# Performance work log

Measured on AMD Instinct MI355X. Metric: run time of the kernel, lower is better.

Reference implementation:

```python
import jax, jax.numpy as jnp
import numpy as np

GRID = 128      # voxel grid extent per axis
NUM_BATCH = 4
N_PER = 25000   # points per scene (unique voxels)
C = 128
K = 32          # number of classes in probs
HEADS = 8
SCALE = 1.0


def setup_inputs() -> dict:
    key = jax.random.key(0)
    ks = jax.random.split(key, 12)
    N = NUM_BATCH * N_PER
    # unique voxel coordinates per scene (submanifold conv assumes no duplicate sites)
    coords_list = []
    for b in range(NUM_BATCH):
        flat = jax.random.permutation(jax.random.fold_in(ks[0], b), GRID ** 3)[:N_PER]
        xyz = jnp.stack([flat // (GRID * GRID), (flat // GRID) % GRID, flat % GRID], axis=1)
        bcol = jnp.full((N_PER, 1), b)
        coords_list.append(jnp.concatenate([bcol, xyz], axis=1))
    coords = jnp.concatenate(coords_list, axis=0).astype(jnp.int32)  # [N,4] = (b,x,y,z)
    feats = jax.random.normal(ks[1], (N, C), jnp.float32)
    probs = jax.random.normal(ks[2], (N, K), jnp.float32)
    conv_w = jax.random.normal(ks[3], (27, C, C), jnp.float32) * (1.0 / np.sqrt(27 * C))
    bn_gamma = 1.0 + 0.1 * jax.random.normal(ks[4], (C,), jnp.float32)
    bn_beta = 0.1 * jax.random.normal(ks[5], (C,), jnp.float32)
    in_proj_w = jax.random.normal(ks[6], (3 * C, C), jnp.float32) / np.sqrt(C)
    in_proj_b = 0.01 * jax.random.normal(ks[7], (3 * C,), jnp.float32)
    out_proj_w = jax.random.normal(ks[8], (C, C), jnp.float32) / np.sqrt(C)
    out_proj_b = 0.01 * jax.random.normal(ks[9], (C,), jnp.float32)
    bottleneck_w = jax.random.normal(ks[10], (C, 2 * C), jnp.float32) / np.sqrt(2 * C)
    return {"feats": feats, "probs": probs, "conv_w": conv_w, "bn_gamma": bn_gamma,
            "bn_beta": bn_beta, "in_proj_w": in_proj_w, "in_proj_b": in_proj_b,
            "out_proj_w": out_proj_w, "out_proj_b": out_proj_b,
            "bottleneck_w": bottleneck_w, "coords": coords, "batch_size": NUM_BATCH}


def _subm_conv3x3(feats, coords, conv_w, batch_size):
    """Submanifold 3x3x3 sparse conv: outputs only at active sites, gathering active neighbors."""
    N = feats.shape[0]
    b, xyz = coords[:, 0], coords[:, 1:]
    grid = jnp.full((batch_size, GRID, GRID, GRID), -1, jnp.int32)
    grid = grid.at[b, xyz[:, 0], xyz[:, 1], xyz[:, 2]].set(jnp.arange(N, dtype=jnp.int32))
    out = jnp.zeros((N, conv_w.shape[-1]), feats.dtype)
    kidx = 0
    for dx in (-1, 0, 1):
        for dy in (-1, 0, 1):
            for dz in (-1, 0, 1):
                nb = xyz + jnp.array([dx, dy, dz], jnp.int32)
                inb = jnp.all((nb >= 0) & (nb < GRID), axis=1)
                nbc = jnp.clip(nb, 0, GRID - 1)
                j = grid[b, nbc[:, 0], nbc[:, 1], nbc[:, 2]]
                ok = inb & (j >= 0)
                g = jnp.where(ok[:, None], feats[jnp.maximum(j, 0)], 0.0)
                out = out + g @ conv_w[kidx]
                kidx += 1
    return out


def _forward(feats, probs, conv_w, bn_gamma, bn_beta, in_proj_w, in_proj_b,
             out_proj_w, out_proj_b, bottleneck_w, coords, batch_size):
    N, Cc = feats.shape
    dh = Cc // HEADS
    b = coords[:, 0]
    # transform_input: SubMConv3d -> BatchNorm1d (batch stats) -> ReLU
    x = _subm_conv3x3(feats, coords, conv_w, batch_size)
    mu = jnp.mean(x, axis=0)
    var = jnp.var(x, axis=0)
    x = jax.nn.relu((x - mu) * jax.lax.rsqrt(var + 1e-5) * bn_gamma + bn_beta)
    # SpatialGatherModule: per-scene softmax over points, soft-weighted context [B,K,C]
    m = b[None, :] == jnp.arange(batch_size, dtype=b.dtype)[:, None]          # [B,N]
    neg = jnp.finfo(x.dtype).min
    z = jnp.where(m[:, :, None], (SCALE * probs)[None], neg)                  # [B,N,K]
    w = jax.nn.softmax(z, axis=1)
    ctx = jnp.einsum('bnk,nc->bkc', w, x)                                     # [B,K,C]
    # per-scene MultiheadAttention (unbatched): query = points, key/value = context
    Wq, Wk, Wv = in_proj_w[:Cc], in_proj_w[Cc:2 * Cc], in_proj_w[2 * Cc:]
    bq, bk, bv = in_proj_b[:Cc], in_proj_b[Cc:2 * Cc], in_proj_b[2 * Cc:]
    q = ((x @ Wq.T + bq) * (dh ** -0.5)).reshape(N, HEADS, dh)
    kh = (ctx @ Wk.T + bk).reshape(batch_size, -1, HEADS, dh)
    vh = (ctx @ Wv.T + bv).reshape(batch_size, -1, HEADS, dh)
    scores = jnp.einsum('nhd,bkhd->nbhk', q, kh)
    scores = scores[jnp.arange(N), b]                                         # [N,H,K] pick own scene
    attn = jax.nn.softmax(scores, axis=-1)
    o = jnp.einsum('nhk,bkhd->nbhd', attn, vh)[jnp.arange(N), b]              # [N,H,dh]
    attn_out = o.reshape(N, Cc) @ out_proj_w.T + out_proj_b
    # torch code aliases feats with inputs.features, so the in-place scatter makes
    # both halves of the concat equal to attn_out (literal forward semantics)
    y = jnp.concatenate([attn_out, attn_out], axis=1) @ bottleneck_w.T
    return y


def reference(feats, probs, conv_w, bn_gamma, bn_beta, in_proj_w, in_proj_b,
              out_proj_w, out_proj_b, bottleneck_w, coords, batch_size):
    return _forward(feats, probs, conv_w, bn_gamma, bn_beta, in_proj_w, in_proj_b,
                    out_proj_w, out_proj_b, bottleneck_w, coords, batch_size)
```

## Files before the change

### kernel.cpp

```cpp
#include <hip/hip_runtime.h>
#include <hip/hip_bf16.h>

typedef __attribute__((ext_vector_type(8))) short short8;
typedef __attribute__((ext_vector_type(4))) float floatx4;

#define NB 4
#define GRIDD 128
#define GRID3 (128*128*128)
#define C 128
#define KSLOT 32
#define CTX_BPB 256
#define DEN_BLK 1024
#define STAT_BLK 1024
#define PCAP 8192

static __device__ __forceinline__ unsigned short f2bf(float f){
  unsigned u = __builtin_bit_cast(unsigned, f);
  unsigned r = (u + 0x7FFFu + ((u >> 16) & 1u)) >> 16;
  return (unsigned short)r;
}
static __device__ __forceinline__ float bf2f(unsigned short h){
  unsigned u = ((unsigned)h) << 16;
  return __builtin_bit_cast(float, u);
}

__global__ void prepk(const float* __restrict__ feats, const float* __restrict__ convw,
                      const float* __restrict__ inw,
                      unsigned short* __restrict__ Fb, unsigned short* __restrict__ Wt,
                      unsigned short* __restrict__ Wq, unsigned short* __restrict__ WkvT,
                      long total1)
{
  const long stride = (long)gridDim.x * blockDim.x;
  const long i0 = (long)blockIdx.x * blockDim.x + threadIdx.x;
  const long q4 = total1 >> 2;
  const float4* f4 = reinterpret_cast<const float4*>(feats);
  ushort4* fb4 = reinterpret_cast<ushort4*>(Fb);
  for (long i = i0; i < q4; i += stride){
    const float4 v = f4[i];
    ushort4 o; o.x = f2bf(v.x); o.y = f2bf(v.y); o.z = f2bf(v.z); o.w = f2bf(v.w);
    fb4[i] = o;
  }
  for (long i = i0; i < 27L*C*C; i += stride){
    long k = i >> 14; long r = (i >> 7) & 127; long c = i & 127;
    Wt[i] = f2bf(convw[(k << 14) + (c << 7) + r]);
  }
  for (long i = i0; i < C*C; i += stride) Wq[i] = f2bf(inw[i]);
  for (long i = i0; i < 2L*C*C; i += stride){
    long which = i >> 14, rem = i & 16383, ii = rem >> 7, cout = rem & 127;
    WkvT[i] = f2bf(inw[((1 + which) << 14) + (cout << 7) + ii]);
  }
}

__global__ __launch_bounds__(128) void w2k(const float* __restrict__ bw,
                                           const float* __restrict__ outw,
                                           const float* __restrict__ outb,
                                           unsigned short* __restrict__ W2b,
                                           float* __restrict__ b2){
  const int o = blockIdx.x, i = threadIdx.x;
  __shared__ float wcf[128];
  __shared__ float red[128];
  const float w_i = bw[(size_t)o*256 + i] + bw[(size_t)o*256 + 128 + i];
  wcf[i] = w_i;
  red[i] = w_i * outb[i];
  __syncthreads();
  float acc = 0.f;
  #pragma unroll 8
  for (int j = 0; j < 128; j++) acc = fmaf(wcf[j], outw[j*128 + i], acc);
  W2b[o*128 + i] = f2bf(acc);
  for (int s = 64; s > 0; s >>= 1){
    if (i < s) red[i] += red[i + s];
    __syncthreads();
  }
  if (i == 0) b2[o] = red[0];
}

__global__ void scatterk(const int* __restrict__ coords, int* __restrict__ gh, int N){
  int p = blockIdx.x * 256 + threadIdx.x;
  if (p < N){
    int4 cr = *reinterpret_cast<const int4*>(coords + (size_t)p * 4);
    gh[(((cr.x*GRIDD + cr.y)*GRIDD + cr.z)*GRIDD) + cr.w] = p;
  }
}

__global__ __launch_bounds__(256) void pairk(const int* __restrict__ coords,
                                             const int* __restrict__ gh,
                                             int2* __restrict__ pairs,
                                             int* __restrict__ gcnt, int N){
  __shared__ int wcnt[4][27];
  __shared__ int woff[4][27];
  const int t = threadIdx.x, wave = t >> 6, lane = t & 63;
  const int p = blockIdx.x * 256 + t;
  const bool active = p < N;
  int4 cr = make_int4(0, 0, 0, 0);
  if (active) cr = *reinterpret_cast<const int4*>(coords + (size_t)p * 4);
  const int b = cr.x, x = cr.y, y = cr.z, z = cr.w;
  int jl[27];
  #pragma unroll
  for (int k = 0; k < 27; k++){
    jl[k] = -1;
    if (k == 13) continue;
    if (active){
      const int dx = k / 9 - 1, dy = (k / 3) % 3 - 1, dz = k % 3 - 1;
      const int nx = x + dx, ny = y + dy, nz = z + dz;
      if (((unsigned)nx < 128u) & ((unsigned)ny < 128u) & ((unsigned)nz < 128u)){
        const int gi = ((((b << 7) + nx) << 7) + ny) * GRIDD + nz;
        const int jj = gh[gi];
        if ((unsigned)jj < (unsigned)N){
          const int4 cj = *reinterpret_cast<const int4*>(coords + (size_t)jj * 4);
          if (cj.x == b && cj.y == nx && cj.z == ny && cj.w == nz) jl[k] = jj;
        }
      }
    }
  }
  #pragma unroll
  for (int k = 0; k < 27; k++){
    const unsigned long long m = __ballot(jl[k] >= 0);
    if (lane == 0) wcnt[wave][k] = (int)__popcll(m);
  }
  __syncthreads();
  if (t < 27){
    const int c0 = wcnt[0][t], c1 = wcnt[1][t], c2 = wcnt[2][t], c3 = wcnt[3][t];
    const int tot = c0 + c1 + c2 + c3;
    int gb = 0;
    if (t != 13 && tot > 0) gb = atomicAdd(&gcnt[t], tot);
    woff[0][t] = gb;
    woff[1][t] = gb + c0;
    woff[2][t] = gb + c0 + c1;
    woff[3][t] = gb + c0 + c1 + c2;
  }
  __syncthreads();
  const unsigned long long ltm = ((unsigned long long)1 << lane) - 1;
  #pragma unroll
  for (int k = 0; k < 27; k++){
    if (k == 13) continue;
    const unsigned long long m = __ballot(jl[k] >= 0);
    if (jl[k] >= 0){
      const int slot = woff[wave][k] + (int)__popcll(m & ltm);
      if (slot < PCAP) pairs[(size_t)k * PCAP + slot] = make_int2(p, jl[k]);
    }
  }
}

__global__ __launch_bounds__(256) void scatk(
    const unsigned short* __restrict__ F, const unsigned short* __restrict__ Wt,
    const int2* __restrict__ pairs, const int* __restrict__ gcnt,
    float* __restrict__ X, int N)
{
  __shared__ unsigned short wl[128 * 136];
  const int k = (blockIdx.x < 13) ? blockIdx.x : blockIdx.x + 1;
  const int t = threadIdx.x;
  const unsigned short* wg = Wt + (size_t)k * C * C;
  for (int idx = t; idx < 128 * 16; idx += 256){
    const int row = idx >> 4, seg = idx & 15;
    *reinterpret_cast<short8*>(&wl[row * 136 + seg * 8]) =
        *reinterpret_cast<const short8*>(wg + row * 128 + seg * 8);
  }
  __syncthreads();
  const int cnt = min(gcnt[k], PCAP);
  const int nch = (cnt + 15) >> 4;
  const int wave = t >> 6, lane = t & 63, lo = lane & 15, hi = lane >> 4;
  for (int c = blockIdx.y * 4 + wave; c < nch; c += 32 * 4){
    const int pidx = c * 16 + lo;
    const bool pv = pidx < cnt;
    const int2 pr = pv ? pairs[(size_t)k * PCAP + pidx] : make_int2(0, 0);
    const unsigned short* frow = F + (size_t)pr.y * C;
    short8 a[4];
    #pragma unroll
    for (int kc = 0; kc < 4; kc++){
      a[kc] = *reinterpret_cast<const short8*>(frow + kc * 32 + hi * 8);
      if (!pv) a[kc] = (short8){0,0,0,0,0,0,0,0};
    }
    floatx4 acc[8];
    #pragma unroll
    for (int i = 0; i < 8; i++) acc[i] = (floatx4){0.f,0.f,0.f,0.f};
    #pragma unroll
    for (int kc = 0; kc < 4; kc++){
      const int koff = kc * 32 + hi * 8;
      #pragma unroll
      for (int ct = 0; ct < 8; ct++){
        const short8 b = *reinterpret_cast<const short8*>(&wl[(ct*16 + lo) * 136 + koff]);
        acc[ct] = __builtin_amdgcn_mfma_f32_16x16x32_bf16(a[kc], b, acc[ct], 0, 0, 0);
      }
    }
    #pragma unroll
    for (int i2 = 0; i2 < 4; i2++){
      const int src = hi * 4 + i2;
      const int row = __shfl(pr.x, src);
      if (c * 16 + src < cnt){
        #pragma unroll
        for (int ct = 0; ct < 8; ct++)
          atomicAdd(&X[(size_t)row * C + ct * 16 + lo], acc[ct][i2]);
      }
    }
  }
}

__global__ __launch_bounds__(256) void denomk(const float* __restrict__ probs,
                                              const int* __restrict__ coords,
                                              float* __restrict__ dpart,
                                              float* __restrict__ wexp, int N){
  const int t = threadIdx.x, k = t & 31, rh = t >> 5;
  float a0 = 0.f, a1 = 0.f, a2 = 0.f, a3 = 0.f;
  for (int r = blockIdx.x * 8 + rh; r < N; r += DEN_BLK * 8){
    const int b = coords[(size_t)r * 4];
    const float e = __expf(probs[(size_t)r * 32 + k]);
    wexp[(size_t)r * 32 + k] = e;
    a0 += (b == 0) ? e : 0.f;
    a1 += (b == 1) ? e : 0.f;
    a2 += (b == 2) ? e : 0.f;
    a3 += (b == 3) ? e : 0.f;
  }
  __shared__ float ls[8][128];
  ls[rh][0*32 + k] = a0; ls[rh][1*32 + k] = a1;
  ls[rh][2*32 + k] = a2; ls[rh][3*32 + k] = a3;
  __syncthreads();
  if (t < 128){
    float s = 0.f;
    #pragma unroll
    for (int j = 0; j < 8; j++) s += ls[j][t];
    dpart[(size_t)blockIdx.x * 128 + t] = s;
  }
}

__global__ __launch_bounds__(256) void statsk(const float* __restrict__ X,
                                              float* __restrict__ spgs, int N){
  const int t = threadIdx.x, c4 = t & 31, rg = t >> 5;
  float s0=0.f,s1=0.f,s2=0.f,s3=0.f, q0=0.f,q1=0.f,q2=0.f,q3=0.f;
  for (int r = blockIdx.x * 8 + rg; r < N; r += STAT_BLK * 8){
    const float4 v = *reinterpret_cast<const float4*>(X + (size_t)r * C + c4 * 4);
    s0 += v.x; s1 += v.y; s2 += v.z; s3 += v.w;
    q0 = fmaf(v.x, v.x, q0); q1 = fmaf(v.y, v.y, q1);
    q2 = fmaf(v.z, v.z, q2); q3 = fmaf(v.w, v.w, q3);
  }
  __shared__ float ls[256][4], lq[256][4];
  ls[t][0]=s0; ls[t][1]=s1; ls[t][2]=s2; ls[t][3]=s3;
  lq[t][0]=q0; lq[t][1]=q1; lq[t][2]=q2; lq[t][3]=q3;
  __syncthreads();
  if (t < 32){
    float as[4]={0.f,0.f,0.f,0.f}, aq[4]={0.f,0.f,0.f,0.f};
    #pragma unroll
    for (int g = 0; g < 8; g++){
      #pragma unroll
      for (int j = 0; j < 4; j++){ as[j] += ls[g*32 + t][j]; aq[j] += lq[g*32 + t][j]; }
    }
    #pragma unroll
    for (int j = 0; j < 4; j++){
      spgs[(size_t)blockIdx.x * 256 + t*4 + j] = as[j];
      spgs[(size_t)blockIdx.x * 256 + 128 + t*4 + j] = aq[j];
    }
  }
}

__global__ __launch_bounds__(128) void reduk(const float* __restrict__ pgs,
                                             const float* __restrict__ dpart,
                                             float* __restrict__ gsum,
                                             float* __restrict__ gsq,
                                             float* __restrict__ denom){
  const int which = blockIdx.x, slice = blockIdx.y, t = threadIdx.x;
  float s = 0.f;
  if (which < 2){
    const float* src = pgs + which * 128 + t;
    for (int j = slice; j < STAT_BLK; j += 8) s += src[(size_t)j * 256];
    atomicAdd((which ? gsq : gsum) + t, s);
  } else {
    const float* src = dpart + t;
    for (int j = slice; j < DEN_BLK; j += 8) s += src[(size_t)j * 128];
    atomicAdd(denom + t, s);
  }
}

__global__ void finalizek(const float* __restrict__ sums, const float* __restrict__ sumsq,
                          const float* __restrict__ gamma, const float* __restrict__ beta,
                          const float* __restrict__ denom,
                          float* __restrict__ scalev, float* __restrict__ shiftv,
                          float* __restrict__ invden, int N){
  const int t = threadIdx.x;
  const float invN = 1.f / (float)N;
  const float mu = sums[t] * invN;
  const float var = sumsq[t] * invN - mu * mu;
  const float sc = gamma[t] * rsqrtf(var + 1e-5f);
  scalev[t] = sc;
  shiftv[t] = beta[t] - mu * sc;
  invden[t] = 1.f / denom[t];
}

__global__ __launch_bounds__(256) void ctx2k(const float* __restrict__ Xm,
                                             const float* __restrict__ wexp,
                                             const float* __restrict__ scalev,
                                             const float* __restrict__ shiftv,
                                             float* __restrict__ pbuf, int NPER){
  const int blk = blockIdx.x;
  const int b = blk >> 8, j = blk & 255;
  const int rows = (NPER + CTX_BPB - 1) / CTX_BPB;
  const int r0 = j * rows;
  const int r1 = min(r0 + rows, NPER);
  const int t = threadIdx.x, c = t & 127, rh = t >> 7;
  const float sc = scalev[c], sh = shiftv[c];
  float acc[KSLOT];
  #pragma unroll
  for (int k = 0; k < KSLOT; k++) acc[k] = 0.f;
  for (int r = r0 + rh; r < r1; r += 2){
    const size_t nn = (size_t)b * NPER + r;
    const float xv = fmaxf(fmaf(Xm[nn * C + c], sc, sh), 0.f);
    const float4* wr = reinterpret_cast<const float4*>(wexp + nn * KSLOT);
    #pragma unroll
    for (int kq = 0; kq < 8; kq++){
      const float4 w4 = wr[kq];
      acc[kq*4+0] = fmaf(w4.x, xv, acc[kq*4+0]);
      acc[kq*4+1] = fmaf(w4.y, xv, acc[kq*4+1]);
      acc[kq*4+2] = fmaf(w4.z, xv, acc[kq*4+2]);
      acc[kq*4+3] = fmaf(w4.w, xv, acc[kq*4+3]);
    }
  }
  __shared__ float red[2 * KSLOT * C];
  #pragma unroll
  for (int k = 0; k < KSLOT; k++) red[(rh * KSLOT + k) * C + c] = acc[k];
  __syncthreads();
  float* dst = pbuf + (size_t)blk * KSLOT * C;
  for (int i = t; i < KSLOT * C; i += 256) dst[i] = red[i] + red[KSLOT * C + i];
}

__global__ __launch_bounds__(256) void kvk(const float* __restrict__ pbuf,
                                           const float* __restrict__ invden,
                                           const unsigned short* __restrict__ WkvT,
                                           const float* __restrict__ inb,
                                           float* __restrict__ kh, float* __restrict__ vh){
  __shared__ float rowp[2][C];
  __shared__ float row[C];
  const int bk = blockIdx.x;
  const int b = bk >> 5, k = bk & 31;
  const int t = threadIdx.x, c = t & 127, jh = t >> 7;
  float s = 0.f;
  for (int j = jh; j < CTX_BPB; j += 2)
    s += pbuf[((size_t)(b * CTX_BPB + j) * KSLOT + k) * C + c];
  rowp[jh][c] = s;
  __syncthreads();
  if (t < C) row[t] = (rowp[0][t] + rowp[1][t]) * invden[b * KSLOT + k];
  __syncthreads();
  const int which = t >> 7;
  const unsigned short* W = WkvT + (size_t)which * C * C;
  float acc = inb[(1 + which) * C + c];
  #pragma unroll 8
  for (int i = 0; i < C; i++) acc = fmaf(row[i], bf2f(W[i * C + c]), acc);
  (which ? vh : kh)[(size_t)bk * C + c] = acc;
}

__global__ __launch_bounds__(256) void gemm128(
    const unsigned short* __restrict__ A, const unsigned short* __restrict__ W,
    const float* __restrict__ bias, float scale,
    float* __restrict__ outF, unsigned short* __restrict__ outB, int N)
{
  const int tid = threadIdx.x;
  const int wave = tid >> 6, lane = tid & 63;
  const int rbase = blockIdx.x * 64 + (wave >> 1) * 32;
  const int cbase = (wave & 1) * 64;
  const int lo = lane & 15, hi = lane >> 4;
  floatx4 acc[2][4];
  #pragma unroll
  for (int rt = 0; rt < 2; rt++)
    #pragma unroll
    for (int ct = 0; ct < 4; ct++) acc[rt][ct] = (floatx4){0.f,0.f,0.f,0.f};
  const int m0 = rbase + lo, m1 = rbase + 16 + lo;
  const int m0c = m0 < N ? m0 : N - 1;
  const int m1c = m1 < N ? m1 : N - 1;
  #pragma unroll
  for (int kc = 0; kc < 4; kc++){
    const int koff = kc * 32 + hi * 8;
    const short8 a0 = *reinterpret_cast<const short8*>(A + (size_t)m0c * C + koff);
    const short8 a1 = *reinterpret_cast<const short8*>(A + (size_t)m1c * C + koff);
    #pragma unroll
    for (int ct = 0; ct < 4; ct++){
      const int n = cbase + ct * 16 + lo;
      const short8 b = *reinterpret_cast<const short8*>(W + (size_t)n * C + koff);
      acc[0][ct] = __builtin_amdgcn_mfma_f32_16x16x32_bf16(a0, b, acc[0][ct], 0, 0, 0);
      acc[1][ct] = __builtin_amdgcn_mfma_f32_16x16x32_bf16(a1, b, acc[1][ct], 0, 0, 0);
    }
  }
  #pragma unroll
  for (int rt = 0; rt < 2; rt++){
    #pragma unroll
    for (int ct = 0; ct < 4; ct++){
      const int col = cbase + ct * 16 + lo;
      const float bv = bias ? bias[col] : 0.f;
      #pragma unroll
      for (int i = 0; i < 4; i++){
        const int row = rbase + rt * 16 + hi * 4 + i;
        if (row < N){
          const float v = (acc[rt][ct][i] + bv) * scale;
          if (outF) outF[(size_t)row * C + col] = v;
          if (outB) outB[(size_t)row * C + col] = f2bf(v);
        }
      }
    }
  }
}

__global__ __launch_bounds__(256) void gemm128f(
    const float* __restrict__ A, const unsigned short* __restrict__ W,
    const float* __restrict__ bias, const float* __restrict__ bnsc,
    const float* __restrict__ bnsh, float scale,
    unsigned short* __restrict__ outB, int N)
{
  const int tid = threadIdx.x;
  const int wave = tid >> 6, lane = tid & 63;
  const int rbase = blockIdx.x * 64 + (wave >> 1) * 32;
  const int cbase = (wave & 1) * 64;
  const int lo = lane & 15, hi = lane >> 4;
  floatx4 acc[2][4];
  #pragma unroll
  for (int rt = 0; rt < 2; rt++)
    #pragma unroll
    for (int ct = 0; ct < 4; ct++) acc[rt][ct] = (floatx4){0.f,0.f,0.f,0.f};
  const int m0 = rbase + lo, m1 = rbase + 16 + lo;
  const int m0c = m0 < N ? m0 : N - 1;
  const int m1c = m1 < N ? m1 : N - 1;
  #pragma unroll
  for (int kc = 0; kc < 4; kc++){
    const int koff = kc * 32 + hi * 8;
    short8 a0, a1;
    #pragma unroll
    for (int half = 0; half < 2; half++){
      const float4 sc = *reinterpret_cast<const float4*>(bnsc + koff + half * 4);
      const float4 sh = *reinterpret_cast<const float4*>(bnsh + koff + half * 4);
      const float4 x0 = *reinterpret_cast<const float4*>(A + (size_t)m0c * C + koff + half * 4);
      const float4 x1 = *reinterpret_cast<const float4*>(A + (size_t)m1c * C + koff + half * 4);
      const float* scp = &sc.x; const float* shp = &sh.x;
      const float* x0p = &x0.x; const float* x1p = &x1.x;
      #pragma unroll
      for (int j = 0; j < 4; j++){
        a0[half*4 + j] = (short)f2bf(fmaxf(fmaf(x0p[j], scp[j], shp[j]), 0.f));
        a1[half*4 + j] = (short)f2bf(fmaxf(fmaf(x1p[j], scp[j], shp[j]), 0.f));
      }
    }
    #pragma unroll
    for (int ct = 0; ct < 4; ct++){
      const int n = cbase + ct * 16 + lo;
      const short8 b = *reinterpret_cast<const short8*>(W + (size_t)n * C + koff);
      acc[0][ct] = __builtin_amdgcn_mfma_f32_16x16x32_bf16(a0, b, acc[0][ct], 0, 0, 0);
      acc[1][ct] = __builtin_amdgcn_mfma_f32_16x16x32_bf16(a1, b, acc[1][ct], 0, 0, 0);
    }
  }
  #pragma unroll
  for (int rt = 0; rt < 2; rt++){
    #pragma unroll
    for (int ct = 0; ct < 4; ct++){
      const int col = cbase + ct * 16 + lo;
      const float bv = bias[col];
      #pragma unroll
      for (int i = 0; i < 4; i++){
        const int row = rbase + rt * 16 + hi * 4 + i;
        if (row < N) outB[(size_t)row * C + col] = f2bf((acc[rt][ct][i] + bv) * scale);
      }
    }
  }
}

__global__ __launch_bounds__(256) void attn3k(const unsigned short* __restrict__ qb,
                                              const float* __restrict__ kh,
                                              const float* __restrict__ vh,
                                              unsigned short* __restrict__ ob, int NPER){
  __shared__ float khL[KSLOT * C];
  __shared__ float vhL[KSLOT * C];
  const int t = threadIdx.x;
  const int b = blockIdx.y;
  const int n0 = blockIdx.x * 32;
  {
    const float4* ks = reinterpret_cast<const float4*>(kh + (size_t)b * KSLOT * C);
    const float4* vs = reinterpret_cast<const float4*>(vh + (size_t)b * KSLOT * C);
    float4* kd = reinterpret_cast<float4*>(khL);
    float4* vd = reinterpret_cast<float4*>(vhL);
    #pragma unroll
    for (int i = 0; i < 4; i++){ kd[i * 256 + t] = ks[i * 256 + t]; vd[i * 256 + t] = vs[i * 256 + t]; }
  }
  __syncthreads();
  const int h = t >> 5, p = t & 31;
  const int n = n0 + p;
  const int nc = n < NPER ? n : NPER - 1;
  float qv[16];
  {
    const short8* qp = reinterpret_cast<const short8*>(qb + ((size_t)b * NPER + nc) * C + h * 16);
    const short8 qa = qp[0], qc = qp[1];
    #pragma unroll
    for (int i = 0; i < 8; i++){
      qv[i]     = bf2f((unsigned short)qa[i]);
      qv[8 + i] = bf2f((unsigned short)qc[i]);
    }
  }
  float sv[KSLOT];
  #pragma unroll
  for (int k = 0; k < KSLOT; k++){
    const float4* kp = reinterpret_cast<const float4*>(&khL[k * C + h * 16]);
    const float4 k0 = kp[0], k1 = kp[1], k2 = kp[2], k3 = kp[3];
    float s;
    s = qv[0] * k0.x;
    s = fmaf(qv[1], k0.y, s);  s = fmaf(qv[2],  k0.z, s);  s = fmaf(qv[3],  k0.w, s);
    s = fmaf(qv[4], k1.x, s);  s = fmaf(qv[5],  k1.y, s);  s = fmaf(qv[6],  k1.z, s);
    s = fmaf(qv[7], k1.w, s);  s = fmaf(qv[8],  k2.x, s);  s = fmaf(qv[9],  k2.y, s);
    s = fmaf(qv[10], k2.z, s); s = fmaf(qv[11], k2.w, s);  s = fmaf(qv[12], k3.x, s);
    s = fmaf(qv[13], k3.y, s); s = fmaf(qv[14], k3.z, s);  s = fmaf(qv[15], k3.w, s);
    sv[k] = s;
  }
  float m = sv[0];
  #pragma unroll
  for (int k = 1; k < KSLOT; k++) m = fmaxf(m, sv[k]);
  float sum = 0.f;
  #pragma unroll
  for (int k = 0; k < KSLOT; k++){ const float e = __expf(sv[k] - m); sv[k] = e; sum += e; }
  const float inv = 1.f / sum;
  float o[16];
  #pragma unroll
  for (int i = 0; i < 16; i++) o[i] = 0.f;
  #pragma unroll
  for (int k = 0; k < KSLOT; k++){
    const float w = sv[k];
    const float4* vp = reinterpret_cast<const float4*>(&vhL[k * C + h * 16]);
    const float4 v0 = vp[0], v1 = vp[1], v2 = vp[2], v3 = vp[3];
    o[0]  = fmaf(w, v0.x, o[0]);  o[1]  = fmaf(w, v0.y, o[1]);
    o[2]  = fmaf(w, v0.z, o[2]);  o[3]  = fmaf(w, v0.w, o[3]);
    o[4]  = fmaf(w, v1.x, o[4]);  o[5]  = fmaf(w, v1.y, o[5]);
    o[6]  = fmaf(w, v1.z, o[6]);  o[7]  = fmaf(w, v1.w, o[7]);
    o[8]  = fmaf(w, v2.x, o[8]);  o[9]  = fmaf(w, v2.y, o[9]);
    o[10] = fmaf(w, v2.z, o[10]); o[11] = fmaf(w, v2.w, o[11]);
    o[12] = fmaf(w, v3.x, o[12]); o[13] = fmaf(w, v3.y, o[13]);
    o[14] = fmaf(w, v3.z, o[14]); o[15] = fmaf(w, v3.w, o[15]);
  }
  if (n < NPER){
    short8 s0, s1;
    #pragma unroll
    for (int i = 0; i < 8; i++){
      s0[i] = (short)f2bf(o[i] * inv);
      s1[i] = (short)f2bf(o[8 + i] * inv);
    }
    unsigned short* op = ob + ((size_t)b * NPER + n) * C + h * 16;
    *reinterpret_cast<short8*>(op) = s0;
    *reinterpret_cast<short8*>(op + 8) = s1;
  }
}

extern "C" void kernel_launch(void* const* d_in, const int* in_sizes, int n_in,
                              void* d_out, int out_size, void* d_ws, size_t ws_size,
                              hipStream_t stream){
  const float* feats  = (const float*)d_in[0];
  const float* probs  = (const float*)d_in[1];
  const float* convw  = (const float*)d_in[2];
  const float* gamma  = (const float*)d_in[3];
  const float* beta   = (const float*)d_in[4];
  const float* inw    = (const float*)d_in[5];
  const float* inb    = (const float*)d_in[6];
  const float* outw   = (const float*)d_in[7];
  const float* outb   = (const float*)d_in[8];
  const float* bw     = (const float*)d_in[9];
  const int*   coords = (const int*)d_in[10];
  const int N = in_sizes[0] / C;
  const int NPER = N / NB;
  const int NBLK = (N + 63) / 64;

  char* ws = (char*)d_ws;
  size_t off = 0;
  auto alloc = [&](size_t bytes) -> char* {
    char* r = ws + off; off += (bytes + 255) & ~(size_t)255; return r;
  };
  int* grid_h            = (int*)alloc((size_t)NB * GRID3 * 4);
  unsigned short* featsb = (unsigned short*)alloc((size_t)N * C * 2);
  unsigned short* convwt = (unsigned short*)alloc((size_t)27 * C * C * 2);
  unsigned short* wq     = (unsigned short*)alloc((size_t)C * C * 2);
  unsigned short* wkvT   = (unsigned short*)alloc((size_t)2 * C * C * 2);
  unsigned short* w2b    = (unsigned short*)alloc((size_t)C * C * 2);
  float* b2              = (float*)alloc(512);
  float* xconv           = (float*)alloc((size_t)N * C * 4);
  unsigned short* qb     = (unsigned short*)alloc((size_t)N * C * 2);
  int2* pairs            = (int2*)alloc((size_t)27 * PCAP * 8);
  float* spgs            = (float*)alloc((size_t)STAT_BLK * 256 * 4);
  float* dpart           = (float*)alloc((size_t)DEN_BLK * 128 * 4);
  float* zero_base       = (float*)alloc((size_t)512 * 4);
  float* gsum   = zero_base;
  float* gsq    = zero_base + 128;
  float* denom  = zero_base + 256;
  int*   gcnt   = (int*)(zero_base + 384);
  float* invden = (float*)alloc(512);
  float* scalev = (float*)alloc(512);
  float* shiftv = (float*)alloc(512);
  float* kh     = (float*)alloc((size_t)NB * KSLOT * C * 4);
  float* vh     = (float*)alloc((size_t)NB * KSLOT * C * 4);
  float* wexp = (float*)grid_h;
  float* pbuf = wexp + (size_t)N * KSLOT;
  unsigned short* o_bf = featsb;

  const long total1 = (long)N * C;
  (void)hipMemsetAsync(zero_base, 0, (size_t)512 * 4, stream);
  prepk<<<2048, 256, 0, stream>>>(feats, convw, inw, featsb, convwt, wq, wkvT, total1);
  w2k<<<128, 128, 0, stream>>>(bw, outw, outb, w2b, b2);
  scatterk<<<(N + 255) / 256, 256, 0, stream>>>(coords, grid_h, N);
  pairk<<<(N + 255) / 256, 256, 0, stream>>>(coords, grid_h, pairs, gcnt, N);
  denomk<<<DEN_BLK, 256, 0, stream>>>(probs, coords, dpart, wexp, N);
  gemm128<<<NBLK, 256, 0, stream>>>(featsb, convwt + 13 * C * C, nullptr, 1.f, xconv, nullptr, N);
  scatk<<<dim3(26, 32), 256, 0, stream>>>(featsb, convwt, pairs, gcnt, xconv, N);
  statsk<<<STAT_BLK, 256, 0, stream>>>(xconv, spgs, N);
  {
    dim3 rg(3, 8);
    reduk<<<rg, 128, 0, stream>>>(spgs, dpart, gsum, gsq, denom);
  }
  finalizek<<<1, 128, 0, stream>>>(gsum, gsq, gamma, beta, denom, scalev, shiftv, invden, N);
  ctx2k<<<NB * CTX_BPB, 256, 0, stream>>>(xconv, wexp, scalev, shiftv, pbuf, NPER);
  kvk<<<NB * KSLOT, 256, 0, stream>>>(pbuf, invden, wkvT, inb, kh, vh);
  gemm128f<<<NBLK, 256, 0, stream>>>(xconv, wq, inb, scalev, shiftv, 0.25f, qb, N);
  dim3 agrid((NPER + 31) / 32, NB);
  attn3k<<<agrid, 256, 0, stream>>>(qb, kh, vh, o_bf, NPER);
  gemm128<<<NBLK, 256, 0, stream>>>(o_bf, w2b, b2, 1.f, (float*)d_out, nullptr, N);
}
```

Before: 473.9 us.

## Recompute exp(probs) in ctx2k, stage tiles in LDS, double attn rows per block

```diff
diff --git a/kernel.cpp b/kernel.cpp
--- a/kernel.cpp
+++ b/kernel.cpp
@@ -197,14 +197,12 @@
 
 __global__ __launch_bounds__(256) void denomk(const float* __restrict__ probs,
                                               const int* __restrict__ coords,
-                                              float* __restrict__ dpart,
-                                              float* __restrict__ wexp, int N){
+                                              float* __restrict__ dpart, int N){
   const int t = threadIdx.x, k = t & 31, rh = t >> 5;
   float a0 = 0.f, a1 = 0.f, a2 = 0.f, a3 = 0.f;
   for (int r = blockIdx.x * 8 + rh; r < N; r += DEN_BLK * 8){
     const int b = coords[(size_t)r * 4];
     const float e = __expf(probs[(size_t)r * 32 + k]);
-    wexp[(size_t)r * 32 + k] = e;
     a0 += (b == 0) ? e : 0.f;
     a1 += (b == 1) ? e : 0.f;
     a2 += (b == 2) ? e : 0.f;
@@ -285,10 +283,13 @@
 }
 
 __global__ __launch_bounds__(256) void ctx2k(const float* __restrict__ Xm,
-                                             const float* __restrict__ wexp,
+                                             const float* __restrict__ probs,
                                              const float* __restrict__ scalev,
                                              const float* __restrict__ shiftv,
                                              float* __restrict__ pbuf, int NPER){
+  __shared__ float xL[32 * 128];
+  __shared__ float pe[32 * 32];
+  __shared__ float red[2 * KSLOT * C];
   const int blk = blockIdx.x;
   const int b = blk >> 8, j = blk & 255;
   const int rows = (NPER + CTX_BPB - 1) / CTX_BPB;
@@ -299,20 +300,44 @@
   float acc[KSLOT];
   #pragma unroll
   for (int k = 0; k < KSLOT; k++) acc[k] = 0.f;
-  for (int r = r0 + rh; r < r1; r += 2){
-    const size_t nn = (size_t)b * NPER + r;
-    const float xv = fmaxf(fmaf(Xm[nn * C + c], sc, sh), 0.f);
-    const float4* wr = reinterpret_cast<const float4*>(wexp + nn * KSLOT);
-    #pragma unroll
-    for (int kq = 0; kq < 8; kq++){
-      const float4 w4 = wr[kq];
-      acc[kq*4+0] = fmaf(w4.x, xv, acc[kq*4+0]);
-      acc[kq*4+1] = fmaf(w4.y, xv, acc[kq*4+1]);
-      acc[kq*4+2] = fmaf(w4.z, xv, acc[kq*4+2]);
-      acc[kq*4+3] = fmaf(w4.w, xv, acc[kq*4+3]);
-    }
-  }
-  __shared__ float red[2 * KSLOT * C];
+
+  for (int base = r0; base < r1; base += 32){
+    __syncthreads();
+    #pragma unroll
+    for (int i = 0; i < 4; i++){
+      const int idx = i * 256 + t;
+      const int r = idx >> 5, c4 = idx & 31;
+      const int rr = base + r;
+      float4 v = make_float4(0.f, 0.f, 0.f, 0.f);
+      if (rr < r1) v = *reinterpret_cast<const float4*>(Xm + ((size_t)b * NPER + rr) * C + c4 * 4);
+      *reinterpret_cast<float4*>(&xL[r * 128 + c4 * 4]) = v;
+    }
+    {
+      const int r = t >> 3, k4 = t & 7;
+      const int rr = base + r;
+      float4 v = make_float4(0.f, 0.f, 0.f, 0.f);
+      if (rr < r1){
+        const float4 pv = *reinterpret_cast<const float4*>(probs + ((size_t)b * NPER + rr) * 32 + k4 * 4);
+        v.x = __expf(pv.x); v.y = __expf(pv.y); v.z = __expf(pv.z); v.w = __expf(pv.w);
+      }
+      *reinterpret_cast<float4*>(&pe[r * 32 + k4 * 4]) = v;
+    }
+    __syncthreads();
+    const int rend = min(32, r1 - base);
+    for (int r = rh; r < rend; r += 2){
+      const float xv = fmaxf(fmaf(xL[r * 128 + c], sc, sh), 0.f);
+      const float4* wr = reinterpret_cast<const float4*>(&pe[r * 32]);
+      #pragma unroll
+      for (int kq = 0; kq < 8; kq++){
+        const float4 w4 = wr[kq];
+        acc[kq*4+0] = fmaf(w4.x, xv, acc[kq*4+0]);
+        acc[kq*4+1] = fmaf(w4.y, xv, acc[kq*4+1]);
+        acc[kq*4+2] = fmaf(w4.z, xv, acc[kq*4+2]);
+        acc[kq*4+3] = fmaf(w4.w, xv, acc[kq*4+3]);
+      }
+    }
+  }
+  __syncthreads();
   #pragma unroll
   for (int k = 0; k < KSLOT; k++) red[(rh * KSLOT + k) * C + c] = acc[k];
   __syncthreads();
@@ -463,7 +488,7 @@
   __shared__ float vhL[KSLOT * C];
   const int t = threadIdx.x;
   const int b = blockIdx.y;
-  const int n0 = blockIdx.x * 32;
+  const int n0 = blockIdx.x * 64;
   {
     const float4* ks = reinterpret_cast<const float4*>(kh + (size_t)b * KSLOT * C);
     const float4* vs = reinterpret_cast<const float4*>(vh + (size_t)b * KSLOT * C);
@@ -474,66 +499,68 @@
   }
   __syncthreads();
   const int h = t >> 5, p = t & 31;
-  const int n = n0 + p;
-  const int nc = n < NPER ? n : NPER - 1;
-  float qv[16];
-  {
-    const short8* qp = reinterpret_cast<const short8*>(qb + ((size_t)b * NPER + nc) * C + h * 16);
-    const short8 qa = qp[0], qc = qp[1];
-    #pragma unroll
-    for (int i = 0; i < 8; i++){
-      qv[i]     = bf2f((unsigned short)qa[i]);
-      qv[8 + i] = bf2f((unsigned short)qc[i]);
-    }
-  }
-  float sv[KSLOT];
-  #pragma unroll
-  for (int k = 0; k < KSLOT; k++){
-    const float4* kp = reinterpret_cast<const float4*>(&khL[k * C + h * 16]);
-    const float4 k0 = kp[0], k1 = kp[1], k2 = kp[2], k3 = kp[3];
-    float s;
-    s = qv[0] * k0.x;
-    s = fmaf(qv[1], k0.y, s);  s = fmaf(qv[2],  k0.z, s);  s = fmaf(qv[3],  k0.w, s);
-    s = fmaf(qv[4], k1.x, s);  s = fmaf(qv[5],  k1.y, s);  s = fmaf(qv[6],  k1.z, s);
-    s = fmaf(qv[7], k1.w, s);  s = fmaf(qv[8],  k2.x, s);  s = fmaf(qv[9],  k2.y, s);
-    s = fmaf(qv[10], k2.z, s); s = fmaf(qv[11], k2.w, s);  s = fmaf(qv[12], k3.x, s);
-    s = fmaf(qv[13], k3.y, s); s = fmaf(qv[14], k3.z, s);  s = fmaf(qv[15], k3.w, s);
-    sv[k] = s;
-  }
-  float m = sv[0];
-  #pragma unroll
-  for (int k = 1; k < KSLOT; k++) m = fmaxf(m, sv[k]);
-  float sum = 0.f;
-  #pragma unroll
-  for (int k = 0; k < KSLOT; k++){ const float e = __expf(sv[k] - m); sv[k] = e; sum += e; }
-  const float inv = 1.f / sum;
-  float o[16];
-  #pragma unroll
-  for (int i = 0; i < 16; i++) o[i] = 0.f;
-  #pragma unroll
-  for (int k = 0; k < KSLOT; k++){
-    const float w = sv[k];
-    const float4* vp = reinterpret_cast<const float4*>(&vhL[k * C + h * 16]);
-    const float4 v0 = vp[0], v1 = vp[1], v2 = vp[2], v3 = vp[3];
-    o[0]  = fmaf(w, v0.x, o[0]);  o[1]  = fmaf(w, v0.y, o[1]);
-    o[2]  = fmaf(w, v0.z, o[2]);  o[3]  = fmaf(w, v0.w, o[3]);
-    o[4]  = fmaf(w, v1.x, o[4]);  o[5]  = fmaf(w, v1.y, o[5]);
-    o[6]  = fmaf(w, v1.z, o[6]);  o[7]  = fmaf(w, v1.w, o[7]);
-    o[8]  = fmaf(w, v2.x, o[8]);  o[9]  = fmaf(w, v2.y, o[9]);
-    o[10] = fmaf(w, v2.z, o[10]); o[11] = fmaf(w, v2.w, o[11]);
-    o[12] = fmaf(w, v3.x, o[12]); o[13] = fmaf(w, v3.y, o[13]);
-    o[14] = fmaf(w, v3.z, o[14]); o[15] = fmaf(w, v3.w, o[15]);
-  }
-  if (n < NPER){
-    short8 s0, s1;
-    #pragma unroll
-    for (int i = 0; i < 8; i++){
-      s0[i] = (short)f2bf(o[i] * inv);
-      s1[i] = (short)f2bf(o[8 + i] * inv);
-    }
-    unsigned short* op = ob + ((size_t)b * NPER + n) * C + h * 16;
-    *reinterpret_cast<short8*>(op) = s0;
-    *reinterpret_cast<short8*>(op + 8) = s1;
+  for (int g = 0; g < 2; g++){
+    const int n = n0 + g * 32 + p;
+    const int nc = n < NPER ? n : NPER - 1;
+    float qv[16];
+    {
+      const short8* qp = reinterpret_cast<const short8*>(qb + ((size_t)b * NPER + nc) * C + h * 16);
+      const short8 qa = qp[0], qc = qp[1];
+      #pragma unroll
+      for (int i = 0; i < 8; i++){
+        qv[i]     = bf2f((unsigned short)qa[i]);
+        qv[8 + i] = bf2f((unsigned short)qc[i]);
+      }
+    }
+    float sv[KSLOT];
+    #pragma unroll
+    for (int k = 0; k < KSLOT; k++){
+      const float4* kp = reinterpret_cast<const float4*>(&khL[k * C + h * 16]);
+      const float4 k0 = kp[0], k1 = kp[1], k2 = kp[2], k3 = kp[3];
+      float s;
+      s = qv[0] * k0.x;
+      s = fmaf(qv[1], k0.y, s);  s = fmaf(qv[2],  k0.z, s);  s = fmaf(qv[3],  k0.w, s);
+      s = fmaf(qv[4], k1.x, s);  s = fmaf(qv[5],  k1.y, s);  s = fmaf(qv[6],  k1.z, s);
+      s = fmaf(qv[7], k1.w, s);  s = fmaf(qv[8],  k2.x, s);  s = fmaf(qv[9],  k2.y, s);
+      s = fmaf(qv[10], k2.z, s); s = fmaf(qv[11], k2.w, s);  s = fmaf(qv[12], k3.x, s);
+      s = fmaf(qv[13], k3.y, s); s = fmaf(qv[14], k3.z, s);  s = fmaf(qv[15], k3.w, s);
+      sv[k] = s;
+    }
+    float m = sv[0];
+    #pragma unroll
+    for (int k = 1; k < KSLOT; k++) m = fmaxf(m, sv[k]);
+    float sum = 0.f;
+    #pragma unroll
+    for (int k = 0; k < KSLOT; k++){ const float e = __expf(sv[k] - m); sv[k] = e; sum += e; }
+    const float inv = 1.f / sum;
+    float o[16];
+    #pragma unroll
+    for (int i = 0; i < 16; i++) o[i] = 0.f;
+    #pragma unroll
+    for (int k = 0; k < KSLOT; k++){
+      const float w = sv[k];
+      const float4* vp = reinterpret_cast<const float4*>(&vhL[k * C + h * 16]);
+      const float4 v0 = vp[0], v1 = vp[1], v2 = vp[2], v3 = vp[3];
+      o[0]  = fmaf(w, v0.x, o[0]);  o[1]  = fmaf(w, v0.y, o[1]);
+      o[2]  = fmaf(w, v0.z, o[2]);  o[3]  = fmaf(w, v0.w, o[3]);
+      o[4]  = fmaf(w, v1.x, o[4]);  o[5]  = fmaf(w, v1.y, o[5]);
+      o[6]  = fmaf(w, v1.z, o[6]);  o[7]  = fmaf(w, v1.w, o[7]);
+      o[8]  = fmaf(w, v2.x, o[8]);  o[9]  = fmaf(w, v2.y, o[9]);
+      o[10] = fmaf(w, v2.z, o[10]); o[11] = fmaf(w, v2.w, o[11]);
+      o[12] = fmaf(w, v3.x, o[12]); o[13] = fmaf(w, v3.y, o[13]);
+      o[14] = fmaf(w, v3.z, o[14]); o[15] = fmaf(w, v3.w, o[15]);
+    }
+    if (n < NPER){
+      short8 s0, s1;
+      #pragma unroll
+      for (int i = 0; i < 8; i++){
+        s0[i] = (short)f2bf(o[i] * inv);
+        s1[i] = (short)f2bf(o[8 + i] * inv);
+      }
+      unsigned short* op = ob + ((size_t)b * NPER + n) * C + h * 16;
+      *reinterpret_cast<short8*>(op) = s0;
+      *reinterpret_cast<short8*>(op + 8) = s1;
+    }
   }
 }
 
@@ -582,17 +609,15 @@
   float* shiftv = (float*)alloc(512);
   float* kh     = (float*)alloc((size_t)NB * KSLOT * C * 4);
   float* vh     = (float*)alloc((size_t)NB * KSLOT * C * 4);
-  float* wexp = (float*)grid_h;
-  float* pbuf = wexp + (size_t)N * KSLOT;
+  float* pbuf = (float*)grid_h;
   unsigned short* o_bf = featsb;
 
-  const long total1 = (long)N * C;
   (void)hipMemsetAsync(zero_base, 0, (size_t)512 * 4, stream);
-  prepk<<<2048, 256, 0, stream>>>(feats, convw, inw, featsb, convwt, wq, wkvT, total1);
+  prepk<<<2048, 256, 0, stream>>>(feats, convw, inw, featsb, convwt, wq, wkvT, (long)N * C);
   w2k<<<128, 128, 0, stream>>>(bw, outw, outb, w2b, b2);
   scatterk<<<(N + 255) / 256, 256, 0, stream>>>(coords, grid_h, N);
   pairk<<<(N + 255) / 256, 256, 0, stream>>>(coords, grid_h, pairs, gcnt, N);
-  denomk<<<DEN_BLK, 256, 0, stream>>>(probs, coords, dpart, wexp, N);
+  denomk<<<DEN_BLK, 256, 0, stream>>>(probs, coords, dpart, N);
   gemm128<<<NBLK, 256, 0, stream>>>(featsb, convwt + 13 * C * C, nullptr, 1.f, xconv, nullptr, N);
   scatk<<<dim3(26, 32), 256, 0, stream>>>(featsb, convwt, pairs, gcnt, xconv, N);
   statsk<<<STAT_BLK, 256, 0, stream>>>(xconv, spgs, N);
@@ -601,10 +626,10 @@
     reduk<<<rg, 128, 0, stream>>>(spgs, dpart, gsum, gsq, denom);
   }
   finalizek<<<1, 128, 0, stream>>>(gsum, gsq, gamma, beta, denom, scalev, shiftv, invden, N);
-  ctx2k<<<NB * CTX_BPB, 256, 0, stream>>>(xconv, wexp, scalev, shiftv, pbuf, NPER);
+  ctx2k<<<NB * CTX_BPB, 256, 0, stream>>>(xconv, probs, scalev, shiftv, pbuf, NPER);
   kvk<<<NB * KSLOT, 256, 0, stream>>>(pbuf, invden, wkvT, inb, kh, vh);
   gemm128f<<<NBLK, 256, 0, stream>>>(xconv, wq, inb, scalev, shiftv, 0.25f, qb, N);
-  dim3 agrid((NPER + 31) / 32, NB);
+  dim3 agrid((NPER + 63) / 64, NB);
   attn3k<<<agrid, 256, 0, stream>>>(qb, kh, vh, o_bf, NPER);
   gemm128<<<NBLK, 256, 0, stream>>>(o_bf, w2b, b2, 1.f, (float*)d_out, nullptr, N);
 }
```

Result: faster. 456.2 us (-3.7%).
